# Performance work log

Measured on AMD Instinct MI355X. Metric: run time of the kernel, lower is better.

## Reference

```python
import jax, jax.numpy as jnp
import numpy as np

B, T, D, H, L = 128, 512, 512, 512, 256


def setup_inputs() -> dict:
    key = jax.random.key(0)
    ks = jax.random.split(key, 7)
    lim = 1.0 / np.sqrt(H)
    u = lambda k, shape, lo: jax.random.uniform(k, shape, jnp.float32, -lo, lo)
    x = jax.random.normal(ks[0], (B, T, D), dtype=jnp.float32)
    Wih = u(ks[1], (3 * H, D), lim)
    Whh = u(ks[2], (3 * H, H), lim)
    b = u(ks[3], (3 * H,), lim)
    bn = u(ks[4], (H,), lim)
    lim_l = 1.0 / np.sqrt(H)
    Wlin = u(ks[5], (2 * L, H), lim_l)
    blin = u(ks[6], (2 * L,), lim_l)
    return {"x": x, "Wih": Wih, "Whh": Whh, "b": b, "bn": bn, "Wlin": Wlin, "blin": blin}


def reference(x, Wih, Whh, b, bn, Wlin, blin):
    # x: (B, T, D). Batched GRU recurrence over time via lax.scan.
    def step(h, xt):
        ig = xt @ Wih.T + b           # (B, 3H)
        hg = h @ Whh.T                # (B, 3H)
        ir, iz, inn = jnp.split(ig, 3, axis=-1)
        hr, hz, hn = jnp.split(hg, 3, axis=-1)
        r = jax.nn.sigmoid(ir + hr)
        z = jax.nn.sigmoid(iz + hz)
        n = jnp.tanh(inn + r * (hn + bn))
        h_new = (1.0 - z) * n + z * h
        return h_new, None

    xs = jnp.swapaxes(x, 0, 1)        # (T, B, D)
    h0 = jnp.zeros((x.shape[0], Whh.shape[1]), dtype=x.dtype)
    h_final, _ = jax.lax.scan(step, h0, xs)
    out = h_final @ Wlin.T + blin     # (B, 2L)
    mu, logvar = jnp.split(out, 2, axis=-1)
    return (mu, logvar)
```

## Files before the change

kernel.cpp:

```cpp
#include <hip/hip_runtime.h>
#include <stdint.h>


typedef short short8 __attribute__((ext_vector_type(8)));
typedef float f32x4 __attribute__((ext_vector_type(4)));
typedef int int4v __attribute__((ext_vector_type(4)));

#define NB 128
#define NT 512
#define ND 512
#define NH 512
#define NG 1536
#define HSLOT (NB * NH)

__device__ __forceinline__ unsigned short f2bf(float f) {
  union { float f; unsigned u; } v; v.f = f;
  unsigned r = v.u + 0x7fffu + ((v.u >> 16) & 1u);
  return (unsigned short)(r >> 16);
}
__device__ __forceinline__ float bf2f(unsigned short u) {
  union { unsigned u; float f; } v; v.u = ((unsigned)u) << 16; return v.f;
}
__device__ __forceinline__ float sigmoid_f(float x) {
  float e = __builtin_amdgcn_exp2f(-1.4426950408889634f * x);
  return __builtin_amdgcn_rcpf(1.0f + e);
}
__device__ __forceinline__ float tanh_f(float x) {
  float e = __builtin_amdgcn_exp2f(2.8853900817779268f * x);
  return 1.0f - 2.0f * __builtin_amdgcn_rcpf(1.0f + e);
}
__device__ __forceinline__ short8 pack8(float4 a, float4 b) {
  short8 s;
  s[0] = (short)f2bf(a.x); s[1] = (short)f2bf(a.y);
  s[2] = (short)f2bf(a.z); s[3] = (short)f2bf(a.w);
  s[4] = (short)f2bf(b.x); s[5] = (short)f2bf(b.y);
  s[6] = (short)f2bf(b.z); s[7] = (short)f2bf(b.w);
  return s;
}

__device__ __forceinline__ void issue4(const unsigned short* r0,
                                       const unsigned short* r1,
                                       const unsigned short* r2,
                                       const unsigned short* r3,
                                       int4v (&v)[4]) {
  asm volatile(
      "global_load_dwordx4 %0, %4, off sc0 sc1\n\t"
      "global_load_dwordx4 %1, %5, off sc0 sc1\n\t"
      "global_load_dwordx4 %2, %6, off sc0 sc1\n\t"
      "global_load_dwordx4 %3, %7, off sc0 sc1"
      : "=&v"(v[0]), "=&v"(v[1]), "=&v"(v[2]), "=&v"(v[3])
      : "v"(r0), "v"(r1), "v"(r2), "v"(r3) : "memory");
}

__device__ __forceinline__ void wait4(int4v (&v)[4]) {
  asm volatile("s_waitcnt vmcnt(0)"
               : "+v"(v[0]), "+v"(v[1]), "+v"(v[2]), "+v"(v[3]) :: "memory");
}

__device__ __forceinline__ int4v load16_s(const unsigned short* p) {
  int4v v;
  asm volatile("global_load_dwordx4 %0, %1, off sc0 sc1\n\t"
               "s_waitcnt vmcnt(0)"
               : "=v"(v) : "v"(p) : "memory");
  return v;
}

__device__ __forceinline__ void store8_nd(unsigned short* p, unsigned long long v) {
  asm volatile("global_store_dwordx2 %0, %1, off sc0 sc1"
               :: "v"(p), "v"(v) : "memory");
}

__device__ __forceinline__ unsigned pkmax(unsigned a, unsigned b) {
  unsigned d;
  asm("v_pk_max_u16 %0, %1, %2" : "=v"(d) : "v"(a), "v"(b));
  return d;
}
__device__ __forceinline__ bool has_sent(int4v v) {
  unsigned m = pkmax(pkmax((unsigned)v[0], (unsigned)v[1]),
                     pkmax((unsigned)v[2], (unsigned)v[3]));
  return ((m & 0xFFFFu) == 0xFFFFu) || ((m >> 16) == 0xFFFFu);
}

__global__ __launch_bounds__(256) void cvt_bf16(
    const float* __restrict__ in, unsigned short* __restrict__ out, int n8) {
  int i = blockIdx.x * blockDim.x + threadIdx.x;
  const int stride = gridDim.x * blockDim.x;
  for (; i < n8; i += stride) {
    float4 a = ((const float4*)in)[2 * i];
    float4 b = ((const float4*)in)[2 * i + 1];
    *(short8*)&out[(size_t)i * 8] = pack8(a, b);
  }
}

__global__ __launch_bounds__(256) void ig_gemm(
    const float* __restrict__ x, const float* __restrict__ Wih,
    const float* __restrict__ bias, unsigned short* __restrict__ IG) {
  __shared__ unsigned short As[128 * 40];
  __shared__ unsigned short Bs[128 * 40];
  const int tid = threadIdx.x;
  const int bn = blockIdx.x, bm = blockIdx.y;
  const int lane = tid & 63, w = tid >> 6;
  const int wm = w >> 1, wn = w & 1;
  const int l15 = lane & 15, q = lane >> 4;

  f32x4 acc[4][4] = {};

  for (int kt = 0; kt < 16; ++kt) {
    __syncthreads();
#pragma unroll
    for (int j = 0; j < 4; ++j) {
      int fi = tid + 256 * j;
      int row = fi >> 3, kq = fi & 7;
      float4 v = *(const float4*)(x + (size_t)(bm * 128 + row) * ND + kt * 32 + kq * 4);
      ushort4 s = {f2bf(v.x), f2bf(v.y), f2bf(v.z), f2bf(v.w)};
      *(ushort4*)&As[row * 40 + kq * 4] = s;
    }
#pragma unroll
    for (int j = 0; j < 4; ++j) {
      int fi = tid + 256 * j;
      int row = fi >> 3, kq = fi & 7;
      float4 v = *(const float4*)(Wih + (size_t)(bn * 128 + row) * ND + kt * 32 + kq * 4);
      ushort4 s = {f2bf(v.x), f2bf(v.y), f2bf(v.z), f2bf(v.w)};
      *(ushort4*)&Bs[row * 40 + kq * 4] = s;
    }
    __syncthreads();

    short8 af[4], bf[4];
#pragma unroll
    for (int tm = 0; tm < 4; ++tm)
      af[tm] = *(const short8*)&As[(wm * 64 + tm * 16 + l15) * 40 + q * 8];
#pragma unroll
    for (int tn = 0; tn < 4; ++tn)
      bf[tn] = *(const short8*)&Bs[(wn * 64 + tn * 16 + l15) * 40 + q * 8];
#pragma unroll
    for (int tm = 0; tm < 4; ++tm)
#pragma unroll
      for (int tn = 0; tn < 4; ++tn)
        acc[tm][tn] = __builtin_amdgcn_mfma_f32_16x16x32_bf16(af[tm], bf[tn], acc[tm][tn], 0, 0, 0);
  }

#pragma unroll
  for (int tm = 0; tm < 4; ++tm) {
#pragma unroll
    for (int tn = 0; tn < 4; ++tn) {
      int col = bn * 128 + wn * 64 + tn * 16 + l15;
      float bb = bias[col];
#pragma unroll
      for (int i = 0; i < 4; ++i) {
        int row = bm * 128 + wm * 64 + tm * 16 + q * 4 + i;
        IG[(size_t)row * NG + col] = f2bf(acc[tm][tn][i] + bb);
      }
    }
  }
}

__global__ __launch_bounds__(256) void ig_gemm_bf16(
    const unsigned short* __restrict__ xb, const unsigned short* __restrict__ wb,
    const float* __restrict__ bias, unsigned short* __restrict__ IG) {
  __shared__ unsigned short As[128 * 40];
  __shared__ unsigned short Bs[128 * 40];
  __shared__ unsigned short Ts[128 * 128];
  const int tid = threadIdx.x;
  const int bn = blockIdx.x, bm = blockIdx.y;
  const int lane = tid & 63, w = tid >> 6;
  const int wm = w >> 1, wn = w & 1;
  const int l15 = lane & 15, q = lane >> 4;

  f32x4 acc[4][4] = {};

  for (int kt = 0; kt < 16; ++kt) {
    __syncthreads();
#pragma unroll
    for (int j = 0; j < 2; ++j) {
      int gi = tid + 256 * j;
      int row = gi >> 2, kq = gi & 3;
      *(short8*)&As[row * 40 + kq * 8] =
          *(const short8*)(xb + (size_t)(bm * 128 + row) * ND + kt * 32 + kq * 8);
    }
#pragma unroll
    for (int j = 0; j < 2; ++j) {
      int gi = tid + 256 * j;
      int row = gi >> 2, kq = gi & 3;
      *(short8*)&Bs[row * 40 + kq * 8] =
          *(const short8*)(wb + (size_t)(bn * 128 + row) * ND + kt * 32 + kq * 8);
    }
    __syncthreads();

    short8 af[4], bf[4];
#pragma unroll
    for (int tm = 0; tm < 4; ++tm)
      af[tm] = *(const short8*)&As[(wm * 64 + tm * 16 + l15) * 40 + q * 8];
#pragma unroll
    for (int tn = 0; tn < 4; ++tn)
      bf[tn] = *(const short8*)&Bs[(wn * 64 + tn * 16 + l15) * 40 + q * 8];
#pragma unroll
    for (int tm = 0; tm < 4; ++tm)
#pragma unroll
      for (int tn = 0; tn < 4; ++tn)
        acc[tm][tn] = __builtin_amdgcn_mfma_f32_16x16x32_bf16(af[tm], bf[tn], acc[tm][tn], 0, 0, 0);
  }

#pragma unroll
  for (int tm = 0; tm < 4; ++tm) {
#pragma unroll
    for (int tn = 0; tn < 4; ++tn) {
      int cl = wn * 64 + tn * 16 + l15;
      float bb = bias[bn * 128 + cl];
#pragma unroll
      for (int i = 0; i < 4; ++i) {
        int rl = wm * 64 + tm * 16 + q * 4 + i;
        Ts[rl * 128 + cl] = f2bf(acc[tm][tn][i] + bb);
      }
    }
  }
  __syncthreads();
#pragma unroll
  for (int j = 0; j < 8; ++j) {
    int gi = tid + 256 * j;
    int row = gi >> 4, c16 = gi & 15;
    *(short8*)(IG + (size_t)(bm * 128 + row) * NG + bn * 128 + c16 * 8) =
        *(const short8*)&Ts[row * 128 + c16 * 8];
  }
}

template <bool USE_IG>
__global__ __launch_bounds__(256, 1) void gru_rec(
    const float* __restrict__ x, const float* __restrict__ Wih,
    const float* __restrict__ Whh, const float* __restrict__ bias,
    const float* __restrict__ bn, const unsigned short* __restrict__ IG,
    unsigned short* __restrict__ hbuf, float* __restrict__ hfin) {
  __shared__ __align__(16) unsigned short hs[16 * 512];
  __shared__ __align__(16) unsigned short ts[16 * 64];

  const int tid = threadIdx.x;
  const int lane = tid & 63;
  const int w = tid >> 6;
  const int l15 = lane & 15, q = lane >> 4;
  const int bid = blockIdx.x;
  const int g = bid & 7, c = bid >> 3;
  const int col = c * 64 + w * 16 + l15;
  const int erow = g * 16 + q * 4;
  const int mrow = g * 16 + l15;

  short8 bfr[3][16];
#pragma unroll
  for (int gt = 0; gt < 3; ++gt) {
    const float* src = Whh + (size_t)(gt * NH + col) * NH + q * 8;
#pragma unroll
    for (int kk = 0; kk < 16; ++kk) {
      float4 v0 = *(const float4*)(src + kk * 32);
      float4 v1 = *(const float4*)(src + kk * 32 + 4);
      bfr[gt][kk] = pack8(v0, v1);
    }
  }

  float bi_r = 0.f, bi_z = 0.f, bi_n = 0.f;
  if (!USE_IG) {
    bi_r = bias[col];
    bi_z = bias[NH + col];
    bi_n = bias[2 * NH + col];
  }
  const float bnv = bn[col];

  float hreg[4] = {0.f, 0.f, 0.f, 0.f};

  const int frow = tid >> 4;
  const int j2 = tid & 15;
  const int fr7 = frow & 7;
  const size_t rowoff = (size_t)(g * 16 + frow) * NH;
  const int e0 = ((j2) ^ fr7) << 3;
  const int e1 = ((j2 + 16) ^ fr7) << 3;
  const int e2 = ((32 + j2) ^ fr7) << 3;
  const int e3 = ((48 + j2) ^ fr7) << 3;

  const int srow = tid >> 4;
  const int scol = (tid & 15) * 4;
  const size_t cell_off = (size_t)(g * 16 + srow) * NH + c * 64 + scol;

  int4v v[4];
  issue4(hbuf + rowoff + e0, hbuf + rowoff + e1,
         hbuf + rowoff + e2, hbuf + rowoff + e3, v);

  for (int t = 0; t < NT; ++t) {
    unsigned short* hnxt  = hbuf + (size_t)((t + 1) & 3) * HSLOT;
    unsigned short* hsent = hbuf + (size_t)((t + 2) & 3) * HSLOT;
    const unsigned short* hrow = hbuf + (size_t)(t & 3) * HSLOT + rowoff;

    float igr[4], igz[4], ign[4];
    if (USE_IG) {
#pragma unroll
      for (int i = 0; i < 4; ++i) {
        const size_t base = ((size_t)(erow + i) * NT + t) * NG + col;
        igr[i] = bf2f(IG[base]);
        igz[i] = bf2f(IG[base + NH]);
        ign[i] = bf2f(IG[base + 2 * NH]);
      }
    }

    wait4(v);
    if (t > 0) {
      while (has_sent(v[0])) v[0] = load16_s(hrow + e0);
      while (has_sent(v[1])) v[1] = load16_s(hrow + e1);
      while (has_sent(v[2])) v[2] = load16_s(hrow + e2);
      while (has_sent(v[3])) v[3] = load16_s(hrow + e3);
    }
    *(int4v*)&hs[frow * 512 + (j2 << 3)] = v[0];
    *(int4v*)&hs[frow * 512 + ((j2 + 16) << 3)] = v[1];
    *(int4v*)&hs[frow * 512 + ((32 + j2) << 3)] = v[2];
    *(int4v*)&hs[frow * 512 + ((48 + j2) << 3)] = v[3];
    __syncthreads();

    if (t + 2 < NT) store8_nd(hsent + cell_off, 0xFFFFFFFFFFFFFFFFull);

    f32x4 ar = {0.f, 0.f, 0.f, 0.f};
    f32x4 az = {0.f, 0.f, 0.f, 0.f};
    f32x4 an = {0.f, 0.f, 0.f, 0.f};
    f32x4 ai = {0.f, 0.f, 0.f, 0.f};
    const int abase = l15 * 512;
    const int ar7 = (l15 & 7) << 3;
#pragma unroll
    for (int kk = 0; kk < 16; ++kk) {
      short8 afk = *(const short8*)&hs[abase + ((kk * 32 + q * 8) ^ ar7)];
      ar = __builtin_amdgcn_mfma_f32_16x16x32_bf16(afk, bfr[0][kk], ar, 0, 0, 0);
      az = __builtin_amdgcn_mfma_f32_16x16x32_bf16(afk, bfr[1][kk], az, 0, 0, 0);
      an = __builtin_amdgcn_mfma_f32_16x16x32_bf16(afk, bfr[2][kk], an, 0, 0, 0);
      if (!USE_IG) {
        const float* xp = x + ((size_t)mrow * NT + t) * ND + kk * 32 + q * 8;
        short8 xa = pack8(*(const float4*)xp, *(const float4*)(xp + 4));
#pragma unroll
        for (int gt = 0; gt < 3; ++gt) {
          const float* wp = Wih + (size_t)(gt * NH + col) * ND + kk * 32 + q * 8;
          short8 wf = pack8(*(const float4*)wp, *(const float4*)(wp + 4));
          if (gt == 0) ar = __builtin_amdgcn_mfma_f32_16x16x32_bf16(xa, wf, ar, 0, 0, 0);
          if (gt == 1) az = __builtin_amdgcn_mfma_f32_16x16x32_bf16(xa, wf, az, 0, 0, 0);
          if (gt == 2) ai = __builtin_amdgcn_mfma_f32_16x16x32_bf16(xa, wf, ai, 0, 0, 0);
        }
      }
    }

    unsigned short sv[4];
#pragma unroll
    for (int i = 0; i < 4; ++i) {
      float xr = USE_IG ? (ar[i] + igr[i]) : (ar[i] + bi_r);
      float xz = USE_IG ? (az[i] + igz[i]) : (az[i] + bi_z);
      float xin = USE_IG ? ign[i] : (ai[i] + bi_n);
      float r = sigmoid_f(xr);
      float z = sigmoid_f(xz);
      float n = tanh_f(xin + r * (an[i] + bnv));
      float hn2 = (1.f - z) * n + z * hreg[i];
      hreg[i] = hn2;
      sv[i] = f2bf(hn2);
      if (t == NT - 1) hfin[(size_t)(erow + i) * NH + col] = hn2;
    }

    if (t != NT - 1) {
#pragma unroll
      for (int i = 0; i < 4; ++i)
        ts[(q * 4 + i) * 64 + w * 16 + l15] = sv[i];
      asm volatile("s_waitcnt vmcnt(0)" ::: "memory");
      __syncthreads();
      store8_nd(hnxt + cell_off,
                *(const unsigned long long*)&ts[srow * 64 + scol]);
      issue4(hnxt + rowoff + e0, hnxt + rowoff + e1,
             hnxt + rowoff + e2, hnxt + rowoff + e3, v);
    }
  }
}

__global__ __launch_bounds__(256) void final_linear(
    const float* __restrict__ hfin, const float* __restrict__ Wlin,
    const float* __restrict__ blin, float* __restrict__ out) {
  __shared__ float sh[16 * 516];
  const int tid = threadIdx.x;
  const int b0 = blockIdx.y * 16, o0 = blockIdx.x * 16;

  for (int j = tid; j < 16 * 128; j += 256) {
    int row = j >> 7, kq = j & 127;
    *(float4*)&sh[row * 516 + kq * 4] =
        *(const float4*)(hfin + (size_t)(b0 + row) * NH + kq * 4);
  }
  __syncthreads();

  const int bi = tid & 15, oi = tid >> 4;
  const int o = o0 + oi;
  const float4* wp = (const float4*)(Wlin + (size_t)o * NH);
  float4 a4 = {0.f, 0.f, 0.f, 0.f};
  for (int k4 = 0; k4 < 128; ++k4) {
    float4 wv = wp[k4];
    float4 hv = *(const float4*)&sh[bi * 516 + k4 * 4];
    a4.x += wv.x * hv.x; a4.y += wv.y * hv.y;
    a4.z += wv.z * hv.z; a4.w += wv.w * hv.w;
  }
  float v = a4.x + a4.y + a4.z + a4.w + blin[o];
  int b = b0 + bi;
  if (o < 256) out[b * 256 + o] = v;
  else out[32768 + b * 256 + (o - 256)] = v;
}

extern "C" void kernel_launch(void* const* d_in, const int* in_sizes, int n_in,
                              void* d_out, int out_size, void* d_ws, size_t ws_size,
                              hipStream_t stream) {
  const float* x    = (const float*)d_in[0];
  const float* Wih  = (const float*)d_in[1];
  const float* Whh  = (const float*)d_in[2];
  const float* bias = (const float*)d_in[3];
  const float* bn   = (const float*)d_in[4];
  const float* Wlin = (const float*)d_in[5];
  const float* blin = (const float*)d_in[6];
  float* out = (float*)d_out;

  char* ws = (char*)d_ws;
  unsigned short* hbuf = (unsigned short*)ws;
  float* hfin          = (float*)(ws + 4 * 131072);
  unsigned short* IG   = (unsigned short*)(ws + 4 * 131072 + 262144);
  const size_t need_min = 4 * 131072 + 262144;
  const size_t need_ig  = need_min + (size_t)NB * NT * NG * 2;
  const size_t need_bf  = need_ig + 67108864ull + 1572864ull;
  unsigned short* xb = (unsigned short*)(ws + need_ig);
  unsigned short* wb = (unsigned short*)(ws + need_ig + 67108864ull);
  if (ws_size < need_min) return;

  hipMemsetAsync(ws, 0, 131072, stream);
  hipMemsetAsync(ws + 131072, 0xFF, 3 * 131072, stream);

  const bool useIG = (ws_size >= need_ig);
  const bool useBF = (ws_size >= need_bf);
  if (useIG) {
    if (useBF) {
      cvt_bf16<<<2048, 256, 0, stream>>>(x, xb, (NB * NT * ND) / 8);
      cvt_bf16<<<384, 256, 0, stream>>>(Wih, wb, (NG * ND) / 8);
      ig_gemm_bf16<<<dim3(12, 512), 256, 0, stream>>>(xb, wb, bias, IG);
    } else {
      ig_gemm<<<dim3(12, 512), 256, 0, stream>>>(x, Wih, bias, IG);
    }
    gru_rec<true><<<64, 256, 0, stream>>>(x, Wih, Whh, bias, bn, IG, hbuf, hfin);
  } else {
    gru_rec<false><<<64, 256, 0, stream>>>(x, Wih, Whh, bias, bn, nullptr, hbuf, hfin);
  }
  final_linear<<<dim3(32, 8), 256, 0, stream>>>(hfin, Wlin, blin, out);
}
```

Before: 1.995 ms.

## Fuse input-gate GEMM with GRU recurrence using time-chunked completion counters

Merges the input-projection GEMM and the recurrent GRU kernel into one persistent launch. 64 blocks run the recurrence while the other 192 blocks compute IG tiles in time-quarter order. Each finished tile bumps a per-quarter atomic counter, and the recurrence polls that counter every 128 steps before it reads IG. This hides most of the GEMM behind the serial recurrence, at the cost of relying on all 256 blocks being co-resident, extra polling, and GEMM traffic competing with the latency-bound recurrence.

```diff
diff --git a/kernel.cpp b/kernel.cpp
--- a/kernel.cpp
+++ b/kernel.cpp
@@ -70,6 +70,18 @@
                :: "v"(p), "v"(v) : "memory");
 }
 
+__device__ __forceinline__ void store16_s(unsigned short* p, int4v v) {
+  asm volatile("global_store_dwordx4 %0, %1, off sc0 sc1"
+               :: "v"(p), "v"(v) : "memory");
+}
+
+__device__ __forceinline__ unsigned poll_s(const unsigned* p) {
+  unsigned f;
+  asm volatile("global_load_dword %0, %1, off sc0 sc1\n\t"
+               "s_waitcnt vmcnt(0)" : "=v"(f) : "v"(p) : "memory");
+  return f;
+}
+
 __device__ __forceinline__ unsigned pkmax(unsigned a, unsigned b) {
   unsigned d;
   asm("v_pk_max_u16 %0, %1, %2" : "=v"(d) : "v"(a), "v"(b));
@@ -154,89 +166,18 @@
   }
 }
 
-__global__ __launch_bounds__(256) void ig_gemm_bf16(
-    const unsigned short* __restrict__ xb, const unsigned short* __restrict__ wb,
-    const float* __restrict__ bias, unsigned short* __restrict__ IG) {
-  __shared__ unsigned short As[128 * 40];
-  __shared__ unsigned short Bs[128 * 40];
-  __shared__ unsigned short Ts[128 * 128];
-  const int tid = threadIdx.x;
-  const int bn = blockIdx.x, bm = blockIdx.y;
-  const int lane = tid & 63, w = tid >> 6;
-  const int wm = w >> 1, wn = w & 1;
-  const int l15 = lane & 15, q = lane >> 4;
-
-  f32x4 acc[4][4] = {};
-
-  for (int kt = 0; kt < 16; ++kt) {
-    __syncthreads();
-#pragma unroll
-    for (int j = 0; j < 2; ++j) {
-      int gi = tid + 256 * j;
-      int row = gi >> 2, kq = gi & 3;
-      *(short8*)&As[row * 40 + kq * 8] =
-          *(const short8*)(xb + (size_t)(bm * 128 + row) * ND + kt * 32 + kq * 8);
-    }
-#pragma unroll
-    for (int j = 0; j < 2; ++j) {
-      int gi = tid + 256 * j;
-      int row = gi >> 2, kq = gi & 3;
-      *(short8*)&Bs[row * 40 + kq * 8] =
-          *(const short8*)(wb + (size_t)(bn * 128 + row) * ND + kt * 32 + kq * 8);
-    }
-    __syncthreads();
-
-    short8 af[4], bf[4];
-#pragma unroll
-    for (int tm = 0; tm < 4; ++tm)
-      af[tm] = *(const short8*)&As[(wm * 64 + tm * 16 + l15) * 40 + q * 8];
-#pragma unroll
-    for (int tn = 0; tn < 4; ++tn)
-      bf[tn] = *(const short8*)&Bs[(wn * 64 + tn * 16 + l15) * 40 + q * 8];
-#pragma unroll
-    for (int tm = 0; tm < 4; ++tm)
-#pragma unroll
-      for (int tn = 0; tn < 4; ++tn)
-        acc[tm][tn] = __builtin_amdgcn_mfma_f32_16x16x32_bf16(af[tm], bf[tn], acc[tm][tn], 0, 0, 0);
-  }
-
-#pragma unroll
-  for (int tm = 0; tm < 4; ++tm) {
-#pragma unroll
-    for (int tn = 0; tn < 4; ++tn) {
-      int cl = wn * 64 + tn * 16 + l15;
-      float bb = bias[bn * 128 + cl];
-#pragma unroll
-      for (int i = 0; i < 4; ++i) {
-        int rl = wm * 64 + tm * 16 + q * 4 + i;
-        Ts[rl * 128 + cl] = f2bf(acc[tm][tn][i] + bb);
-      }
-    }
-  }
-  __syncthreads();
-#pragma unroll
-  for (int j = 0; j < 8; ++j) {
-    int gi = tid + 256 * j;
-    int row = gi >> 4, c16 = gi & 15;
-    *(short8*)(IG + (size_t)(bm * 128 + row) * NG + bn * 128 + c16 * 8) =
-        *(const short8*)&Ts[row * 128 + c16 * 8];
-  }
-}
-
 template <bool USE_IG>
-__global__ __launch_bounds__(256, 1) void gru_rec(
+__device__ __forceinline__ void gru_body(
     const float* __restrict__ x, const float* __restrict__ Wih,
     const float* __restrict__ Whh, const float* __restrict__ bias,
     const float* __restrict__ bn, const unsigned short* __restrict__ IG,
-    unsigned short* __restrict__ hbuf, float* __restrict__ hfin) {
-  __shared__ __align__(16) unsigned short hs[16 * 512];
-  __shared__ __align__(16) unsigned short ts[16 * 64];
-
+    unsigned short* __restrict__ hbuf, float* __restrict__ hfin,
+    const unsigned* __restrict__ qcnt,
+    unsigned short* hs, unsigned short* ts, int bid) {
   const int tid = threadIdx.x;
   const int lane = tid & 63;
   const int w = tid >> 6;
   const int l15 = lane & 15, q = lane >> 4;
-  const int bid = blockIdx.x;
   const int g = bid & 7, c = bid >> 3;
   const int col = c * 64 + w * 16 + l15;
   const int erow = g * 16 + q * 4;
@@ -285,6 +226,15 @@
     unsigned short* hnxt  = hbuf + (size_t)((t + 1) & 3) * HSLOT;
     unsigned short* hsent = hbuf + (size_t)((t + 2) & 3) * HSLOT;
     const unsigned short* hrow = hbuf + (size_t)(t & 3) * HSLOT + rowoff;
+
+    if (USE_IG && qcnt != nullptr && (t & 127) == 0) {
+      if (tid == 0) {
+        const unsigned* qp = qcnt + (t >> 7);
+        unsigned f = poll_s(qp);
+        while (f < 1536u) f = poll_s(qp);
+      }
+      __syncthreads();
+    }
 
     float igr[4], igz[4], ign[4];
     if (USE_IG) {
@@ -367,6 +317,110 @@
   }
 }
 
+template <bool USE_IG>
+__global__ __launch_bounds__(256, 1) void gru_rec(
+    const float* __restrict__ x, const float* __restrict__ Wih,
+    const float* __restrict__ Whh, const float* __restrict__ bias,
+    const float* __restrict__ bn, const unsigned short* __restrict__ IG,
+    unsigned short* __restrict__ hbuf, float* __restrict__ hfin) {
+  __shared__ __align__(16) unsigned short hs[16 * 512];
+  __shared__ __align__(16) unsigned short ts[16 * 64];
+  gru_body<USE_IG>(x, Wih, Whh, bias, bn, IG, hbuf, hfin, nullptr,
+                   hs, ts, blockIdx.x);
+}
+
+__global__ __launch_bounds__(256, 1) void fused_gru_ig(
+    const float* __restrict__ Whh, const float* __restrict__ bn,
+    const unsigned short* __restrict__ xb, const unsigned short* __restrict__ wb,
+    const float* __restrict__ bias, unsigned short* __restrict__ IG,
+    unsigned short* __restrict__ hbuf, float* __restrict__ hfin,
+    unsigned* __restrict__ qcnt) {
+  __shared__ __align__(16) unsigned short hs[16 * 512];
+  __shared__ __align__(16) unsigned short ts[16 * 64];
+  __shared__ __align__(16) unsigned short As[128 * 40];
+  __shared__ __align__(16) unsigned short Bs[128 * 40];
+  __shared__ __align__(16) unsigned short Ts[128 * 128];
+
+  const int bid = blockIdx.x;
+  const int tid = threadIdx.x;
+
+  if (bid < 64) {
+    gru_body<true>(nullptr, nullptr, Whh, bias, bn, IG, hbuf, hfin, qcnt,
+                   hs, ts, bid);
+    return;
+  }
+
+  const int lane = tid & 63, w = tid >> 6;
+  const int wm = w >> 1, wn = w & 1;
+  const int l15 = lane & 15, q = lane >> 4;
+
+  for (int tile = bid - 64; tile < 6144; tile += 192) {
+    const int qq = tile / 1536;
+    const int r = tile - qq * 1536;
+    const int bmq = r / 12, bnn = r - bmq * 12;
+    const int bm = bmq * 4 + qq;
+
+    f32x4 acc[4][4] = {};
+
+    for (int kt = 0; kt < 16; ++kt) {
+      __syncthreads();
+#pragma unroll
+      for (int j = 0; j < 2; ++j) {
+        int gi = tid + 256 * j;
+        int row = gi >> 2, kq = gi & 3;
+        *(short8*)&As[row * 40 + kq * 8] =
+            *(const short8*)(xb + (size_t)(bm * 128 + row) * ND + kt * 32 + kq * 8);
+      }
+#pragma unroll
+      for (int j = 0; j < 2; ++j) {
+        int gi = tid + 256 * j;
+        int row = gi >> 2, kq = gi & 3;
+        *(short8*)&Bs[row * 40 + kq * 8] =
+            *(const short8*)(wb + (size_t)(bnn * 128 + row) * ND + kt * 32 + kq * 8);
+      }
+      __syncthreads();
+
+      short8 af[4], bf[4];
+#pragma unroll
+      for (int tm = 0; tm < 4; ++tm)
+        af[tm] = *(const short8*)&As[(wm * 64 + tm * 16 + l15) * 40 + q * 8];
+#pragma unroll
+      for (int tn = 0; tn < 4; ++tn)
+        bf[tn] = *(const short8*)&Bs[(wn * 64 + tn * 16 + l15) * 40 + q * 8];
+#pragma unroll
+      for (int tm = 0; tm < 4; ++tm)
+#pragma unroll
+        for (int tn = 0; tn < 4; ++tn)
+          acc[tm][tn] = __builtin_amdgcn_mfma_f32_16x16x32_bf16(af[tm], bf[tn], acc[tm][tn], 0, 0, 0);
+    }
+
+#pragma unroll
+    for (int tm = 0; tm < 4; ++tm) {
+#pragma unroll
+      for (int tn = 0; tn < 4; ++tn) {
+        int cl = wn * 64 + tn * 16 + l15;
+        float bb = bias[bnn * 128 + cl];
+#pragma unroll
+        for (int i = 0; i < 4; ++i) {
+          int rl = wm * 64 + tm * 16 + q * 4 + i;
+          Ts[rl * 128 + cl] = f2bf(acc[tm][tn][i] + bb);
+        }
+      }
+    }
+    __syncthreads();
+#pragma unroll
+    for (int j = 0; j < 8; ++j) {
+      int gi = tid + 256 * j;
+      int row = gi >> 4, c16 = gi & 15;
+      store16_s(IG + (size_t)(bm * 128 + row) * NG + bnn * 128 + c16 * 8,
+                *(const int4v*)&Ts[row * 128 + c16 * 8]);
+    }
+    asm volatile("s_waitcnt vmcnt(0)" ::: "memory");
+    __syncthreads();
+    if (tid == 0) atomicAdd(qcnt + qq, 1u);
+  }
+}
+
 __global__ __launch_bounds__(256) void final_linear(
     const float* __restrict__ hfin, const float* __restrict__ Wlin,
     const float* __restrict__ blin, float* __restrict__ out) {
@@ -412,8 +466,9 @@
   char* ws = (char*)d_ws;
   unsigned short* hbuf = (unsigned short*)ws;
   float* hfin          = (float*)(ws + 4 * 131072);
-  unsigned short* IG   = (unsigned short*)(ws + 4 * 131072 + 262144);
-  const size_t need_min = 4 * 131072 + 262144;
+  unsigned* qcnt       = (unsigned*)(ws + 4 * 131072 + 262144);
+  unsigned short* IG   = (unsigned short*)(ws + 4 * 131072 + 262144 + 1024);
+  const size_t need_min = 4 * 131072 + 262144 + 1024;
   const size_t need_ig  = need_min + (size_t)NB * NT * NG * 2;
   const size_t need_bf  = need_ig + 67108864ull + 1572864ull;
   unsigned short* xb = (unsigned short*)(ws + need_ig);
@@ -422,17 +477,17 @@
 
   hipMemsetAsync(ws, 0, 131072, stream);
   hipMemsetAsync(ws + 131072, 0xFF, 3 * 131072, stream);
+  hipMemsetAsync(ws + 4 * 131072 + 262144, 0, 1024, stream);
 
   const bool useIG = (ws_size >= need_ig);
   const bool useBF = (ws_size >= need_bf);
-  if (useIG) {
-    if (useBF) {
-      cvt_bf16<<<2048, 256, 0, stream>>>(x, xb, (NB * NT * ND) / 8);
-      cvt_bf16<<<384, 256, 0, stream>>>(Wih, wb, (NG * ND) / 8);
-      ig_gemm_bf16<<<dim3(12, 512), 256, 0, stream>>>(xb, wb, bias, IG);
-    } else {
-      ig_gemm<<<dim3(12, 512), 256, 0, stream>>>(x, Wih, bias, IG);
-    }
+  if (useIG && useBF) {
+    cvt_bf16<<<2048, 256, 0, stream>>>(x, xb, (NB * NT * ND) / 8);
+    cvt_bf16<<<384, 256, 0, stream>>>(Wih, wb, (NG * ND) / 8);
+    fused_gru_ig<<<256, 256, 0, stream>>>(Whh, bn, xb, wb, bias, IG, hbuf,
+                                          hfin, qcnt);
+  } else if (useIG) {
+    ig_gemm<<<dim3(12, 512), 256, 0, stream>>>(x, Wih, bias, IG);
     gru_rec<true><<<64, 256, 0, stream>>>(x, Wih, Whh, bias, bn, IG, hbuf, hfin);
   } else {
     gru_rec<false><<<64, 256, 0, stream>>>(x, Wih, Whh, bias, bn, nullptr, hbuf, hfin);
```

Measured after the change: 1.899 ms. -4.8%, faster.
